# Kernel tuning notes

Hardware: AMD Instinct MI355X
Metric: run time of the kernel (lower is better)

Reference implementation:

```python
import jax, jax.numpy as jnp
import numpy as np

HIDDEN = 512
ATT = 512
B, S = 32, 2048


def setup_inputs() -> dict:
    key = jax.random.key(0)
    ks = jax.random.split(key, 9)
    enc_output = jax.random.normal(ks[0], (B, S, 2 * HIDDEN), dtype=jnp.float32)
    decoder_hidden = jax.random.normal(ks[1], (B, HIDDEN), dtype=jnp.float32)
    masks = jax.random.randint(ks[2], (B, S, 1), 0, 2).astype(jnp.bool_)
    # Learned params (init_weights style: uniform(-0.1, 0.1), zero bias)
    W_enc = jax.random.uniform(ks[3], (2 * HIDDEN, ATT), minval=-0.1, maxval=0.1, dtype=jnp.float32)
    b_enc = jnp.zeros((ATT,), dtype=jnp.float32)
    W_dec = jax.random.uniform(ks[4], (HIDDEN, ATT), minval=-0.1, maxval=0.1, dtype=jnp.float32)
    b_dec = jnp.zeros((ATT,), dtype=jnp.float32)
    W_att = jax.random.uniform(ks[5], (ATT, 1), minval=-0.1, maxval=0.1, dtype=jnp.float32)
    b_att = jnp.zeros((1,), dtype=jnp.float32)
    return {
        "enc_output": enc_output,
        "decoder_hidden": decoder_hidden,
        "masks": masks,
        "W_enc": W_enc,
        "b_enc": b_enc,
        "W_dec": W_dec,
        "b_dec": b_dec,
        "W_att": W_att,
        "b_att": b_att,
    }


def reference(enc_output, decoder_hidden, masks, W_enc, b_enc, W_dec, b_dec, W_att, b_att):
    # encoder_att: [B, S, A]
    encoder_att = jnp.einsum("bse,ea->bsa", enc_output, W_enc) + b_enc
    # decoder_att: [B, A]
    decoder_att = decoder_hidden @ W_dec + b_dec
    # scores: [B, S, 1]
    scores = jnp.tanh(encoder_att + decoder_att[:, None, :]) @ W_att + b_att
    scores = jnp.where(masks, -jnp.inf, scores)
    att_weights = jax.nn.softmax(scores, axis=1)  # softmax over seq dim
    # context over encoder_att (note: original weights encoder_att, not enc_output)
    att_context_vector = jnp.sum(encoder_att * att_weights, axis=1)  # [B, A]
    return att_context_vector
```

## Files before the change

### kernel.cpp

```cpp
#include <hip/hip_runtime.h>
#include <math.h>

#define B_  32
#define S_  2048
#define E_  1024
#define A_  512
#define H_  512

#define MB   128
#define NCH  (S_ / MB)
#define KT   32
#define NK   (E_ / KT)

typedef __bf16 bf16;
typedef __attribute__((ext_vector_type(8))) __bf16 bf16x8;
typedef __attribute__((ext_vector_type(4))) float  f32x4;

typedef const __attribute__((address_space(1))) unsigned int g_u32;
typedef __attribute__((address_space(3))) unsigned int lds_u32;

__device__ __forceinline__ void glds16(const void* g, void* l) {
    __builtin_amdgcn_global_load_lds((g_u32*)g, (lds_u32*)l, 16, 0, 0);
}

__device__ __forceinline__ float fast_tanh(float x) {
    x = fminf(fmaxf(x, -15.f), 15.f);
    const float e = __expf(2.f * x);
    return (e - 1.f) / (e + 1.f);
}

__global__ __launch_bounds__(256)
void wsplit_kernel(const float* __restrict__ Wenc,
                   bf16* __restrict__ Whi, bf16* __restrict__ Wlo,
                   float* __restrict__ dec_att) {
    __shared__ float tile[64][65];
    const int t  = threadIdx.x;
    const int kb = blockIdx.x >> 3;
    const int ab = blockIdx.x & 7;
    const int k0 = kb * 64, a0 = ab * 64;

    const int di = blockIdx.x * 256 + t;
    if (di < B_ * A_) dec_att[di] = 0.f;

#pragma unroll
    for (int p = 0; p < 8; ++p) {
        const int kk = p * 8 + (t >> 5);
        const int aa = (t & 31) * 2;
        const float2 v = *(const float2*)&Wenc[(size_t)(k0 + kk) * A_ + a0 + aa];
        tile[kk][aa]     = v.x;
        tile[kk][aa + 1] = v.y;
    }
    __syncthreads();

    const int aa  = t >> 2;
    const int kk0 = (t & 3) * 16;
    bf16x8 hv0, hv1, lv0, lv1;
#pragma unroll
    for (int j = 0; j < 16; ++j) {
        const float x = tile[kk0 + j][aa];
        const bf16 h = (bf16)x;
        const bf16 l = (bf16)(x - (float)h);
        if (j < 8) { hv0[j] = h; lv0[j] = l; }
        else       { hv1[j - 8] = h; lv1[j - 8] = l; }
    }
    bf16* dh_ = Whi + (size_t)(a0 + aa) * E_ + k0 + kk0;
    bf16* dl_ = Wlo + (size_t)(a0 + aa) * E_ + k0 + kk0;
    *(bf16x8*)dh_ = hv0; *((bf16x8*)dh_ + 1) = hv1;
    *(bf16x8*)dl_ = lv0; *((bf16x8*)dl_ + 1) = lv1;
}

__global__ __launch_bounds__(256)
void dec_att_kernel(const float* __restrict__ dh,
                    const float* __restrict__ Wdec,
                    const float* __restrict__ bdec,
                    float* __restrict__ dec_att) {
    __shared__ float dhl[64];
    const int b   = blockIdx.x >> 3;
    const int seg = blockIdx.x & 7;
    const int t   = threadIdx.x;
    if (t < 64) dhl[t] = dh[b * H_ + seg * 64 + t];
    __syncthreads();
    const int a0 = t, a1 = t + 256;
    float acc0 = 0.f, acc1 = 0.f;
    const float* Wrow = Wdec + (size_t)(seg * 64) * A_;
#pragma unroll 8
    for (int h = 0; h < 64; ++h) {
        const float s = dhl[h];
        acc0 += s * Wrow[h * A_ + a0];
        acc1 += s * Wrow[h * A_ + a1];
    }
    if (seg == 0) { acc0 += bdec[a0]; acc1 += bdec[a1]; }
    atomicAdd(&dec_att[b * A_ + a0], acc0);
    atomicAdd(&dec_att[b * A_ + a1], acc1);
}

__global__ __launch_bounds__(512, 2)
void fused_kernel(const float* __restrict__ enc,
                  const int*   __restrict__ masks,
                  const bf16*  __restrict__ Whi_g,
                  const bf16*  __restrict__ Wlo_g,
                  const float* __restrict__ benc,
                  const float* __restrict__ Watt,
                  const float* __restrict__ batt,
                  const float* __restrict__ dec_att,
                  float* __restrict__ pm,
                  float* __restrict__ pl,
                  float* __restrict__ pctx) {
    __shared__ __align__(16) bf16 Whi_s[A_ * KT];
    __shared__ __align__(16) bf16 Wlo_s[A_ * KT];
    __shared__ __align__(16) bf16 Ahi_s[MB * KT];
    __shared__ __align__(16) bf16 Alo_s[MB * KT];
    __shared__ float decl[A_], wattl[A_], bencl[A_];
    __shared__ float red[MB * 8];
    __shared__ float score_s[MB], p_s[MB];
    __shared__ int   mask_s[MB];

    const int t    = threadIdx.x;
    const int wv   = t >> 6;
    const int L    = t & 63;
    const int quad = L >> 4;
    const int colL = L & 15;
    const int b    = blockIdx.x >> 4;
    const int ch   = blockIdx.x & 15;
    const int s0   = ch * MB;

    const float* encB = enc + ((size_t)(b * S_ + s0)) * E_;

    f32x4 acc[8][4];
#pragma unroll
    for (int mt = 0; mt < 8; ++mt)
#pragma unroll
        for (int nt = 0; nt < 4; ++nt) acc[mt][nt] = (f32x4){0.f, 0.f, 0.f, 0.f};

    const int arow = t >> 2;
    const int akq  = t & 3;
    const int a_wr = ((arow >> 4) * 512) + akq * 128 +
                     (((arow & 15) ^ (akq << 2)) * 8);
    const float* aptr = encB + (size_t)arow * E_ + akq * 8;
    const int a_rd = quad * 128 + (((L & 15) ^ (quad << 2)) * 8);

    float4 cvA = *(const float4*)(aptr);
    float4 cvB = *(const float4*)(aptr + 4);

    for (int kt = 0; kt < NK; ++kt) {
        const int k0 = kt * KT;
        __syncthreads();

#pragma unroll
        for (int i = 0; i < 4; ++i) {
            const int I = wv * 4 + i;
            const size_t goff = (size_t)(I * 16 + colL) * E_ + k0 + quad * 8;
            glds16(Whi_g + goff, &Whi_s[I * 512]);
            glds16(Wlo_g + goff, &Wlo_s[I * 512]);
        }

        {
            const float xs[8] = {cvA.x, cvA.y, cvA.z, cvA.w,
                                 cvB.x, cvB.y, cvB.z, cvB.w};
            bf16x8 hv, lv;
#pragma unroll
            for (int j = 0; j < 8; ++j) {
                const bf16 h = (bf16)xs[j];
                hv[j] = h;
                lv[j] = (bf16)(xs[j] - (float)h);
            }
            *(bf16x8*)&Ahi_s[a_wr] = hv;
            *(bf16x8*)&Alo_s[a_wr] = lv;
        }

        __syncthreads();

        if (kt + 1 < NK) {
            const float* np = aptr + (kt + 1) * KT;
            cvA = *(const float4*)(np);
            cvB = *(const float4*)(np + 4);
        }

        bf16x8 bh[4], bl[4];
#pragma unroll
        for (int nt = 0; nt < 4; ++nt) {
            bh[nt] = *(const bf16x8*)&Whi_s[(wv * 4 + nt) * 512 + L * 8];
            bl[nt] = *(const bf16x8*)&Wlo_s[(wv * 4 + nt) * 512 + L * 8];
        }
#pragma unroll
        for (int mt = 0; mt < 8; ++mt) {
            const bf16x8 ah = *(const bf16x8*)&Ahi_s[mt * 512 + a_rd];
            const bf16x8 al = *(const bf16x8*)&Alo_s[mt * 512 + a_rd];
#pragma unroll
            for (int nt = 0; nt < 4; ++nt) {
                acc[mt][nt] = __builtin_amdgcn_mfma_f32_16x16x32_bf16(ah, bh[nt], acc[mt][nt], 0, 0, 0);
                acc[mt][nt] = __builtin_amdgcn_mfma_f32_16x16x32_bf16(al, bh[nt], acc[mt][nt], 0, 0, 0);
                acc[mt][nt] = __builtin_amdgcn_mfma_f32_16x16x32_bf16(ah, bl[nt], acc[mt][nt], 0, 0, 0);
            }
        }
    }

    decl[t < A_ ? t : 0]  = dec_att[b * A_ + (t < A_ ? t : 0)];
    wattl[t] = Watt[t];
    bencl[t] = benc[t];
    if (t < MB) mask_s[t] = masks[(size_t)b * S_ + s0 + t];
    __syncthreads();

    float sp[8][4];
#pragma unroll
    for (int mt = 0; mt < 8; ++mt)
#pragma unroll
        for (int r = 0; r < 4; ++r) sp[mt][r] = 0.f;

#pragma unroll
    for (int nt = 0; nt < 4; ++nt) {
        const int cg = wv * 64 + nt * 16 + colL;
        const float bv  = bencl[cg];
        const float dv  = decl[cg];
        const float wav = wattl[cg];
#pragma unroll
        for (int mt = 0; mt < 8; ++mt)
#pragma unroll
            for (int r = 0; r < 4; ++r) {
                const float ea = acc[mt][nt][r] + bv;
                acc[mt][nt][r] = ea;
                sp[mt][r] += fast_tanh(ea + dv) * wav;
            }
    }
#pragma unroll
    for (int d = 1; d < 16; d <<= 1)
#pragma unroll
        for (int mt = 0; mt < 8; ++mt)
#pragma unroll
            for (int r = 0; r < 4; ++r)
                sp[mt][r] += __shfl_xor(sp[mt][r], d);
    if (colL == 0) {
#pragma unroll
        for (int mt = 0; mt < 8; ++mt)
#pragma unroll
            for (int r = 0; r < 4; ++r)
                red[(mt * 16 + quad * 4 + r) * 8 + wv] = sp[mt][r];
    }
    __syncthreads();

    if (t < MB) {
        float s = 0.f;
#pragma unroll
        for (int j = 0; j < 8; ++j) s += red[t * 8 + j];
        score_s[t] = s + batt[0];
    }
    __syncthreads();

    float m_loc = -1e30f;
    for (int r = 0; r < MB; ++r)
        if (!mask_s[r]) m_loc = fmaxf(m_loc, score_s[r]);
    if (t < MB) p_s[t] = mask_s[t] ? 0.f : __expf(score_s[t] - m_loc);
    __syncthreads();

    float ctxl[4] = {0.f, 0.f, 0.f, 0.f};
#pragma unroll
    for (int mt = 0; mt < 8; ++mt)
#pragma unroll
        for (int r = 0; r < 4; ++r) {
            const float p = p_s[mt * 16 + quad * 4 + r];
#pragma unroll
            for (int nt = 0; nt < 4; ++nt) ctxl[nt] += p * acc[mt][nt][r];
        }
#pragma unroll
    for (int nt = 0; nt < 4; ++nt) {
        ctxl[nt] += __shfl_xor(ctxl[nt], 16);
        ctxl[nt] += __shfl_xor(ctxl[nt], 32);
    }
    if (quad == 0) {
#pragma unroll
        for (int nt = 0; nt < 4; ++nt)
            pctx[(size_t)blockIdx.x * A_ + wv * 64 + nt * 16 + colL] = ctxl[nt];
    }
    if (t == 0) {
        float l = 0.f;
        for (int r = 0; r < MB; ++r) l += p_s[r];
        pm[blockIdx.x] = m_loc;
        pl[blockIdx.x] = l;
    }
}

__global__ __launch_bounds__(512)
void combine_kernel(const float* __restrict__ pm,
                    const float* __restrict__ pl,
                    const float* __restrict__ pctx,
                    float* __restrict__ out) {
    const int b = blockIdx.x;
    const int t = threadIdx.x;
    float m_g = -1e30f;
    for (int c = 0; c < NCH; ++c) m_g = fmaxf(m_g, pm[b * NCH + c]);
    float L = 0.f;
    for (int c = 0; c < NCH; ++c)
        L += pl[b * NCH + c] * __expf(pm[b * NCH + c] - m_g);
    const float inv = 1.f / L;
    float s = 0.f;
    for (int c = 0; c < NCH; ++c)
        s += pctx[((size_t)b * NCH + c) * A_ + t] * __expf(pm[b * NCH + c] - m_g);
    out[b * A_ + t] = s * inv;
}

extern "C" void kernel_launch(void* const* d_in, const int* in_sizes, int n_in,
                              void* d_out, int out_size, void* d_ws, size_t ws_size,
                              hipStream_t stream) {
    const float* enc  = (const float*)d_in[0];
    const float* dh   = (const float*)d_in[1];
    const int*   mks  = (const int*)  d_in[2];
    const float* Wenc = (const float*)d_in[3];
    const float* benc = (const float*)d_in[4];
    const float* Wdec = (const float*)d_in[5];
    const float* bdec = (const float*)d_in[6];
    const float* Watt = (const float*)d_in[7];
    const float* batt = (const float*)d_in[8];
    float* out = (float*)d_out;

    float* ws      = (float*)d_ws;
    float* dec_att = ws;
    float* pm      = dec_att + B_ * A_;
    float* pl      = pm + B_ * NCH;
    float* pctx    = pl + B_ * NCH;
    bf16*  Whi     = (bf16*)(pctx + B_ * NCH * A_);
    bf16*  Wlo     = Whi + (size_t)A_ * E_;
    (void)in_sizes; (void)n_in; (void)out_size; (void)ws_size;

    wsplit_kernel<<<128, 256, 0, stream>>>(Wenc, Whi, Wlo, dec_att);
    dec_att_kernel<<<B_ * 8, 256, 0, stream>>>(dh, Wdec, bdec, dec_att);
    fused_kernel<<<B_ * NCH, 512, 0, stream>>>(
        enc, mks, Whi, Wlo, benc, Watt, batt, dec_att, pm, pl, pctx);
    combine_kernel<<<B_, 512, 0, stream>>>(pm, pl, pctx, out);
}
```

Measured before the change: 581.4 us.

## Double-buffer encoder tiles and prefetch weights to overlap loads with MFMA

The main GEMM loop now double-buffers the bf16 hi/lo encoder tiles in LDS. It keeps the current weight fragments in registers, so the global-to-LDS weight loads and the next encoder loads are issued before the MFMAs and overlap with them. Shared memory is unioned between the GEMM phase and the softmax epilogue to keep the footprint within two blocks per CU. The two prep kernels are merged into one launch, and the decoder projection writes per-segment partials that the fused kernel sums, replacing atomics and the zero-init. The cost is extra registers and an added LDS buffer, and it still needs two barriers per iteration.

Result: faster. 523.4 us (-10.0%).

```diff
diff --git a/kernel.cpp b/kernel.cpp
--- a/kernel.cpp
+++ b/kernel.cpp
@@ -30,68 +30,62 @@
 }
 
 __global__ __launch_bounds__(256)
-void wsplit_kernel(const float* __restrict__ Wenc,
-                   bf16* __restrict__ Whi, bf16* __restrict__ Wlo,
-                   float* __restrict__ dec_att) {
-    __shared__ float tile[64][65];
-    const int t  = threadIdx.x;
-    const int kb = blockIdx.x >> 3;
-    const int ab = blockIdx.x & 7;
-    const int k0 = kb * 64, a0 = ab * 64;
-
-    const int di = blockIdx.x * 256 + t;
-    if (di < B_ * A_) dec_att[di] = 0.f;
-
-#pragma unroll
-    for (int p = 0; p < 8; ++p) {
-        const int kk = p * 8 + (t >> 5);
-        const int aa = (t & 31) * 2;
-        const float2 v = *(const float2*)&Wenc[(size_t)(k0 + kk) * A_ + a0 + aa];
-        tile[kk][aa]     = v.x;
-        tile[kk][aa + 1] = v.y;
-    }
-    __syncthreads();
-
-    const int aa  = t >> 2;
-    const int kk0 = (t & 3) * 16;
-    bf16x8 hv0, hv1, lv0, lv1;
-#pragma unroll
-    for (int j = 0; j < 16; ++j) {
-        const float x = tile[kk0 + j][aa];
-        const bf16 h = (bf16)x;
-        const bf16 l = (bf16)(x - (float)h);
-        if (j < 8) { hv0[j] = h; lv0[j] = l; }
-        else       { hv1[j - 8] = h; lv1[j - 8] = l; }
-    }
-    bf16* dh_ = Whi + (size_t)(a0 + aa) * E_ + k0 + kk0;
-    bf16* dl_ = Wlo + (size_t)(a0 + aa) * E_ + k0 + kk0;
-    *(bf16x8*)dh_ = hv0; *((bf16x8*)dh_ + 1) = hv1;
-    *(bf16x8*)dl_ = lv0; *((bf16x8*)dl_ + 1) = lv1;
-}
-
-__global__ __launch_bounds__(256)
-void dec_att_kernel(const float* __restrict__ dh,
-                    const float* __restrict__ Wdec,
-                    const float* __restrict__ bdec,
-                    float* __restrict__ dec_att) {
-    __shared__ float dhl[64];
-    const int b   = blockIdx.x >> 3;
-    const int seg = blockIdx.x & 7;
-    const int t   = threadIdx.x;
-    if (t < 64) dhl[t] = dh[b * H_ + seg * 64 + t];
-    __syncthreads();
-    const int a0 = t, a1 = t + 256;
-    float acc0 = 0.f, acc1 = 0.f;
-    const float* Wrow = Wdec + (size_t)(seg * 64) * A_;
+void prep_kernel(const float* __restrict__ Wenc,
+                 const float* __restrict__ dh,
+                 const float* __restrict__ Wdec,
+                 const float* __restrict__ bdec,
+                 bf16* __restrict__ Whi, bf16* __restrict__ Wlo,
+                 float* __restrict__ dp) {
+    const int t = threadIdx.x;
+    if (blockIdx.x < 128) {
+        __shared__ float tile[64][65];
+        const int kb = blockIdx.x >> 3;
+        const int ab = blockIdx.x & 7;
+        const int k0 = kb * 64, a0 = ab * 64;
+#pragma unroll
+        for (int p = 0; p < 8; ++p) {
+            const int kk = p * 8 + (t >> 5);
+            const int aa = (t & 31) * 2;
+            const float2 v = *(const float2*)&Wenc[(size_t)(k0 + kk) * A_ + a0 + aa];
+            tile[kk][aa]     = v.x;
+            tile[kk][aa + 1] = v.y;
+        }
+        __syncthreads();
+        const int aa  = t >> 2;
+        const int kk0 = (t & 3) * 16;
+        bf16x8 hv0, hv1, lv0, lv1;
+#pragma unroll
+        for (int j = 0; j < 16; ++j) {
+            const float x = tile[kk0 + j][aa];
+            const bf16 h = (bf16)x;
+            const bf16 l = (bf16)(x - (float)h);
+            if (j < 8) { hv0[j] = h; lv0[j] = l; }
+            else       { hv1[j - 8] = h; lv1[j - 8] = l; }
+        }
+        bf16* dh_ = Whi + (size_t)(a0 + aa) * E_ + k0 + kk0;
+        bf16* dl_ = Wlo + (size_t)(a0 + aa) * E_ + k0 + kk0;
+        *(bf16x8*)dh_ = hv0; *((bf16x8*)dh_ + 1) = hv1;
+        *(bf16x8*)dl_ = lv0; *((bf16x8*)dl_ + 1) = lv1;
+    } else {
+        __shared__ float dhl[64];
+        const int idx = blockIdx.x - 128;
+        const int b   = idx >> 3;
+        const int seg = idx & 7;
+        if (t < 64) dhl[t] = dh[b * H_ + seg * 64 + t];
+        __syncthreads();
+        const int a0 = t, a1 = t + 256;
+        float acc0 = 0.f, acc1 = 0.f;
+        const float* Wrow = Wdec + (size_t)(seg * 64) * A_;
 #pragma unroll 8
-    for (int h = 0; h < 64; ++h) {
-        const float s = dhl[h];
-        acc0 += s * Wrow[h * A_ + a0];
-        acc1 += s * Wrow[h * A_ + a1];
-    }
-    if (seg == 0) { acc0 += bdec[a0]; acc1 += bdec[a1]; }
-    atomicAdd(&dec_att[b * A_ + a0], acc0);
-    atomicAdd(&dec_att[b * A_ + a1], acc1);
+        for (int h = 0; h < 64; ++h) {
+            const float s = dhl[h];
+            acc0 += s * Wrow[h * A_ + a0];
+            acc1 += s * Wrow[h * A_ + a1];
+        }
+        if (seg == 0) { acc0 += bdec[a0]; acc1 += bdec[a1]; }
+        dp[(size_t)(seg * B_ + b) * A_ + a0] = acc0;
+        dp[(size_t)(seg * B_ + b) * A_ + a1] = acc1;
+    }
 }
 
 __global__ __launch_bounds__(512, 2)
@@ -102,18 +96,23 @@
                   const float* __restrict__ benc,
                   const float* __restrict__ Watt,
                   const float* __restrict__ batt,
-                  const float* __restrict__ dec_att,
+                  const float* __restrict__ dp,
                   float* __restrict__ pm,
                   float* __restrict__ pl,
                   float* __restrict__ pctx) {
-    __shared__ __align__(16) bf16 Whi_s[A_ * KT];
-    __shared__ __align__(16) bf16 Wlo_s[A_ * KT];
-    __shared__ __align__(16) bf16 Ahi_s[MB * KT];
-    __shared__ __align__(16) bf16 Alo_s[MB * KT];
-    __shared__ float decl[A_], wattl[A_], bencl[A_];
-    __shared__ float red[MB * 8];
-    __shared__ float score_s[MB], p_s[MB];
-    __shared__ int   mask_s[MB];
+    __shared__ union {
+        struct {
+            __align__(16) bf16 Whi[A_ * KT];
+            __align__(16) bf16 Wlo[A_ * KT];
+            __align__(16) bf16 Ab[2][2][MB * KT];
+        } k;
+        struct {
+            float decl[A_], wattl[A_], bencl[A_];
+            float red[MB * 8];
+            float score[MB], p[MB];
+            int   mask[MB];
+        } e;
+    } sm;
 
     const int t    = threadIdx.x;
     const int wv   = t >> 6;
@@ -139,53 +138,60 @@
     const float* aptr = encB + (size_t)arow * E_ + akq * 8;
     const int a_rd = quad * 128 + (((L & 15) ^ (quad << 2)) * 8);
 
-    float4 cvA = *(const float4*)(aptr);
-    float4 cvB = *(const float4*)(aptr + 4);
+    const size_t wg0 = (size_t)((wv * 4) * 16 + colL) * E_ + quad * 8;
+
+    float4 cA = *(const float4*)(aptr);
+    float4 cB = *(const float4*)(aptr + 4);
+#pragma unroll
+    for (int i = 0; i < 4; ++i) {
+        const int I = wv * 4 + i;
+        const size_t goff = wg0 + (size_t)(i * 16) * E_;
+        glds16(Whi_g + goff, &sm.k.Whi[I * 512]);
+        glds16(Wlo_g + goff, &sm.k.Wlo[I * 512]);
+    }
+    {
+        const float xs[8] = {cA.x, cA.y, cA.z, cA.w, cB.x, cB.y, cB.z, cB.w};
+        bf16x8 hv, lv;
+#pragma unroll
+        for (int j = 0; j < 8; ++j) {
+            const bf16 h = (bf16)xs[j];
+            hv[j] = h; lv[j] = (bf16)(xs[j] - (float)h);
+        }
+        *(bf16x8*)&sm.k.Ab[0][0][a_wr] = hv;
+        *(bf16x8*)&sm.k.Ab[0][1][a_wr] = lv;
+    }
+    __syncthreads();
+
+    bf16x8 bh[4], bl[4];
+#pragma unroll
+    for (int nt = 0; nt < 4; ++nt) {
+        bh[nt] = *(const bf16x8*)&sm.k.Whi[(wv * 4 + nt) * 512 + L * 8];
+        bl[nt] = *(const bf16x8*)&sm.k.Wlo[(wv * 4 + nt) * 512 + L * 8];
+    }
 
     for (int kt = 0; kt < NK; ++kt) {
-        const int k0 = kt * KT;
         __syncthreads();
-
-#pragma unroll
-        for (int i = 0; i < 4; ++i) {
-            const int I = wv * 4 + i;
-            const size_t goff = (size_t)(I * 16 + colL) * E_ + k0 + quad * 8;
-            glds16(Whi_g + goff, &Whi_s[I * 512]);
-            glds16(Wlo_g + goff, &Wlo_s[I * 512]);
-        }
-
-        {
-            const float xs[8] = {cvA.x, cvA.y, cvA.z, cvA.w,
-                                 cvB.x, cvB.y, cvB.z, cvB.w};
-            bf16x8 hv, lv;
-#pragma unroll
-            for (int j = 0; j < 8; ++j) {
-                const bf16 h = (bf16)xs[j];
-                hv[j] = h;
-                lv[j] = (bf16)(xs[j] - (float)h);
-            }
-            *(bf16x8*)&Ahi_s[a_wr] = hv;
-            *(bf16x8*)&Alo_s[a_wr] = lv;
-        }
-
-        __syncthreads();
-
-        if (kt + 1 < NK) {
-            const float* np = aptr + (kt + 1) * KT;
-            cvA = *(const float4*)(np);
-            cvB = *(const float4*)(np + 4);
-        }
-
-        bf16x8 bh[4], bl[4];
-#pragma unroll
-        for (int nt = 0; nt < 4; ++nt) {
-            bh[nt] = *(const bf16x8*)&Whi_s[(wv * 4 + nt) * 512 + L * 8];
-            bl[nt] = *(const bf16x8*)&Wlo_s[(wv * 4 + nt) * 512 + L * 8];
-        }
+        const bool more = (kt + 1 < NK);
+        if (more) {
+            const size_t kadd = (size_t)(kt + 1) * KT;
+#pragma unroll
+            for (int i = 0; i < 4; ++i) {
+                const int I = wv * 4 + i;
+                const size_t goff = wg0 + (size_t)(i * 16) * E_ + kadd;
+                glds16(Whi_g + goff, &sm.k.Whi[I * 512]);
+                glds16(Wlo_g + goff, &sm.k.Wlo[I * 512]);
+            }
+            const float* np = aptr + (size_t)(kt + 1) * KT;
+            cA = *(const float4*)(np);
+            cB = *(const float4*)(np + 4);
+        }
+
+        const bf16* Ahi = sm.k.Ab[kt & 1][0];
+        const bf16* Alo = sm.k.Ab[kt & 1][1];
 #pragma unroll
         for (int mt = 0; mt < 8; ++mt) {
-            const bf16x8 ah = *(const bf16x8*)&Ahi_s[mt * 512 + a_rd];
-            const bf16x8 al = *(const bf16x8*)&Alo_s[mt * 512 + a_rd];
+            const bf16x8 ah = *(const bf16x8*)&Ahi[mt * 512 + a_rd];
+            const bf16x8 al = *(const bf16x8*)&Alo[mt * 512 + a_rd];
 #pragma unroll
             for (int nt = 0; nt < 4; ++nt) {
                 acc[mt][nt] = __builtin_amdgcn_mfma_f32_16x16x32_bf16(ah, bh[nt], acc[mt][nt], 0, 0, 0);
@@ -193,12 +199,38 @@
                 acc[mt][nt] = __builtin_amdgcn_mfma_f32_16x16x32_bf16(ah, bl[nt], acc[mt][nt], 0, 0, 0);
             }
         }
-    }
-
-    decl[t < A_ ? t : 0]  = dec_att[b * A_ + (t < A_ ? t : 0)];
-    wattl[t] = Watt[t];
-    bencl[t] = benc[t];
-    if (t < MB) mask_s[t] = masks[(size_t)b * S_ + s0 + t];
+
+        if (more) {
+            const float xs[8] = {cA.x, cA.y, cA.z, cA.w, cB.x, cB.y, cB.z, cB.w};
+            bf16x8 hv, lv;
+#pragma unroll
+            for (int j = 0; j < 8; ++j) {
+                const bf16 h = (bf16)xs[j];
+                hv[j] = h; lv[j] = (bf16)(xs[j] - (float)h);
+            }
+            *(bf16x8*)&sm.k.Ab[(kt + 1) & 1][0][a_wr] = hv;
+            *(bf16x8*)&sm.k.Ab[(kt + 1) & 1][1][a_wr] = lv;
+        }
+
+        __syncthreads();
+        if (more) {
+#pragma unroll
+            for (int nt = 0; nt < 4; ++nt) {
+                bh[nt] = *(const bf16x8*)&sm.k.Whi[(wv * 4 + nt) * 512 + L * 8];
+                bl[nt] = *(const bf16x8*)&sm.k.Wlo[(wv * 4 + nt) * 512 + L * 8];
+            }
+        }
+    }
+
+    {
+        float d = 0.f;
+#pragma unroll
+        for (int g = 0; g < 8; ++g) d += dp[(size_t)(g * B_ + b) * A_ + t];
+        sm.e.decl[t]  = d;
+        sm.e.wattl[t] = Watt[t];
+        sm.e.bencl[t] = benc[t];
+        if (t < MB) sm.e.mask[t] = masks[(size_t)b * S_ + s0 + t];
+    }
     __syncthreads();
 
     float sp[8][4];
@@ -210,9 +242,9 @@
 #pragma unroll
     for (int nt = 0; nt < 4; ++nt) {
         const int cg = wv * 64 + nt * 16 + colL;
-        const float bv  = bencl[cg];
-        const float dv  = decl[cg];
-        const float wav = wattl[cg];
+        const float bv  = sm.e.bencl[cg];
+        const float dv  = sm.e.decl[cg];
+        const float wav = sm.e.wattl[cg];
 #pragma unroll
         for (int mt = 0; mt < 8; ++mt)
 #pragma unroll
@@ -234,22 +266,22 @@
         for (int mt = 0; mt < 8; ++mt)
 #pragma unroll
             for (int r = 0; r < 4; ++r)
-                red[(mt * 16 + quad * 4 + r) * 8 + wv] = sp[mt][r];
+                sm.e.red[(mt * 16 + quad * 4 + r) * 8 + wv] = sp[mt][r];
     }
     __syncthreads();
 
     if (t < MB) {
         float s = 0.f;
 #pragma unroll
-        for (int j = 0; j < 8; ++j) s += red[t * 8 + j];
-        score_s[t] = s + batt[0];
+        for (int j = 0; j < 8; ++j) s += sm.e.red[t * 8 + j];
+        sm.e.score[t] = s + batt[0];
     }
     __syncthreads();
 
     float m_loc = -1e30f;
     for (int r = 0; r < MB; ++r)
-        if (!mask_s[r]) m_loc = fmaxf(m_loc, score_s[r]);
-    if (t < MB) p_s[t] = mask_s[t] ? 0.f : __expf(score_s[t] - m_loc);
+        if (!sm.e.mask[r]) m_loc = fmaxf(m_loc, sm.e.score[r]);
+    if (t < MB) sm.e.p[t] = sm.e.mask[t] ? 0.f : __expf(sm.e.score[t] - m_loc);
     __syncthreads();
 
     float ctxl[4] = {0.f, 0.f, 0.f, 0.f};
@@ -257,7 +289,7 @@
     for (int mt = 0; mt < 8; ++mt)
 #pragma unroll
         for (int r = 0; r < 4; ++r) {
-            const float p = p_s[mt * 16 + quad * 4 + r];
+            const float p = sm.e.p[mt * 16 + quad * 4 + r];
 #pragma unroll
             for (int nt = 0; nt < 4; ++nt) ctxl[nt] += p * acc[mt][nt][r];
         }
@@ -273,7 +305,7 @@
     }
     if (t == 0) {
         float l = 0.f;
-        for (int r = 0; r < MB; ++r) l += p_s[r];
+        for (int r = 0; r < MB; ++r) l += sm.e.p[r];
         pm[blockIdx.x] = m_loc;
         pl[blockIdx.x] = l;
     }
@@ -312,18 +344,17 @@
     const float* batt = (const float*)d_in[8];
     float* out = (float*)d_out;
 
-    float* ws      = (float*)d_ws;
-    float* dec_att = ws;
-    float* pm      = dec_att + B_ * A_;
-    float* pl      = pm + B_ * NCH;
-    float* pctx    = pl + B_ * NCH;
-    bf16*  Whi     = (bf16*)(pctx + B_ * NCH * A_);
-    bf16*  Wlo     = Whi + (size_t)A_ * E_;
+    float* ws   = (float*)d_ws;
+    float* pm   = ws;
+    float* pl   = pm + B_ * NCH;
+    float* pctx = pl + B_ * NCH;
+    float* dp   = pctx + (size_t)B_ * NCH * A_;
+    bf16*  Whi  = (bf16*)(dp + 8 * B_ * A_);
+    bf16*  Wlo  = Whi + (size_t)A_ * E_;
     (void)in_sizes; (void)n_in; (void)out_size; (void)ws_size;
 
-    wsplit_kernel<<<128, 256, 0, stream>>>(Wenc, Whi, Wlo, dec_att);
-    dec_att_kernel<<<B_ * 8, 256, 0, stream>>>(dh, Wdec, bdec, dec_att);
+    prep_kernel<<<384, 256, 0, stream>>>(Wenc, dh, Wdec, bdec, Whi, Wlo, dp);
     fused_kernel<<<B_ * NCH, 512, 0, stream>>>(
-        enc, mks, Whi, Wlo, benc, Watt, batt, dec_att, pm, pl, pctx);
+        enc, mks, Whi, Wlo, benc, Watt, batt, dp, pm, pl, pctx);
     combine_kernel<<<B_, 512, 0, stream>>>(pm, pl, pctx, out);
 }
```
